# Kernel tuning notes

Measured on AMD Instinct MI355X. Metric: run time of the kernel, lower is better.

Reference implementation:

```python
import jax, jax.numpy as jnp
import numpy as np

N_CLUSTERS = 512
TEMPERATURE = 0.1


def setup_inputs() -> dict:
    key = jax.random.key(0)
    k1, k2 = jax.random.split(key)
    x = jax.random.normal(k1, (32, 1024, 256), dtype=jnp.float32)
    centroids = jax.random.normal(k2, (N_CLUSTERS, 256), dtype=jnp.float32)
    return {"x": x, "centroids": centroids}


def reference(x, centroids):
    # Flatten non-cluster axes into a sample axis: [N, D]
    B, S, D = x.shape
    xf = x.reshape(-1, D)  # [N, D]
    x_sq = jnp.sum(xf * xf, axis=-1, keepdims=True)           # [N, 1]
    c_sq = jnp.sum(centroids * centroids, axis=-1)             # [K]
    cross = jnp.einsum('nd,kd->nk', xf, centroids)             # [N, K]
    dists = x_sq - 2.0 * cross + c_sq[None, :]                 # [N, K]
    # Temperature-scaled soft assignments
    assignments = jax.nn.softmax(-dists / TEMPERATURE, axis=-1)  # [N, K]
    # Restore leading (non-feature) dims, append cluster axis
    return assignments.reshape(B, S, N_CLUSTERS)
```

## Files before the change

### kernel.cpp

```cpp
#include <hip/hip_runtime.h>

#define NROWS 32768
#define KC 512
#define DDIM 256
#define BM 64
#define BK 16
#define KCH (DDIM / BK)
#define CHUNK_USH (KC * BK)

typedef __attribute__((ext_vector_type(8)))  short bf16x8;
typedef __attribute__((ext_vector_type(16))) float f32x16;

union U8 { unsigned short u[8]; bf16x8 v; };

__device__ __forceinline__ unsigned short f2bf(float f) {
    union { float f; unsigned int u; } a; a.f = f;
    unsigned int r = a.u + 0x7fffu + ((a.u >> 16) & 1u);
    return (unsigned short)(r >> 16);
}
__device__ __forceinline__ float bf2f(unsigned short h) {
    union { unsigned int u; float f; } a; a.u = ((unsigned int)h) << 16;
    return a.f;
}

__global__ __launch_bounds__(64) void prep_c(const float* __restrict__ c,
                                             unsigned short* __restrict__ bhi,
                                             unsigned short* __restrict__ blo,
                                             float* __restrict__ csq10) {
    const int n = blockIdx.x, lane = threadIdx.x;
    const int d0 = lane * 4;
    float4 v = ((const float4*)(c + (size_t)n * DDIM))[lane];
    float vv[4] = {v.x, v.y, v.z, v.w};
    unsigned short hh[4], ll[4];
    float ssq = 0.f;
    #pragma unroll
    for (int i = 0; i < 4; ++i) {
        ssq += vv[i] * vv[i];
        hh[i] = f2bf(vv[i]);
        ll[i] = f2bf(vv[i] - bf2f(hh[i]));
    }
    #pragma unroll
    for (int off = 32; off; off >>= 1) ssq += __shfl_xor(ssq, off);
    if (lane == 0) csq10[n] = 10.f * ssq;
    const int ks = d0 >> 4;
    const int h  = (d0 >> 3) & 1;
    const int j0 = d0 & 7;
    const size_t dst = (size_t)ks * CHUNK_USH + (n >> 5) * 512 +
                       (h * 32 + (n & 31)) * 8 + j0;
    *(ushort4*)(bhi + dst) = make_ushort4(hh[0], hh[1], hh[2], hh[3]);
    *(ushort4*)(blo + dst) = make_ushort4(ll[0], ll[1], ll[2], ll[3]);
}

__global__ __launch_bounds__(256, 2) void kmeans_mfma(
    const float* __restrict__ x, const unsigned short* __restrict__ bhi,
    const unsigned short* __restrict__ blo, const float* __restrict__ csq10,
    float* __restrict__ out) {
    __shared__ float  lbuf[16 * 516];
    __shared__ float  red0[2][BM], red1[2][BM];
    __shared__ float2 MI[BM];

    const int tid  = threadIdx.x;
    const int w    = tid >> 6, lane = tid & 63;
    const int wm   = w >> 1, wn = w & 1;
    const int c5   = lane & 31, h = lane >> 5;
    const int row0 = blockIdx.x * BM;

    f32x16 acc[8];
    #pragma unroll
    for (int t = 0; t < 8; ++t)
        #pragma unroll
        for (int r = 0; r < 16; ++r) acc[t][r] = 0.f;

    const float* xrow = x + (size_t)(row0 + wm * 32 + c5) * DDIM + h * 8;
    const unsigned short* bhB = bhi + (wn * 8) * 512 + lane * 8;
    const unsigned short* blB = blo + (wn * 8) * 512 + lane * 8;

    for (int ks = 0; ks < KCH; ++ks) {
        const size_t cb = (size_t)ks * CHUNK_USH;
        bf16x8 bh[8], bl[8];
        #pragma unroll
        for (int t = 0; t < 8; ++t) bh[t] = *(const bf16x8*)(bhB + cb + t * 512);
        #pragma unroll
        for (int t = 0; t < 8; ++t) bl[t] = *(const bf16x8*)(blB + cb + t * 512);
        float4 a0 = *(const float4*)(xrow + ks * BK);
        float4 a1 = *(const float4*)(xrow + ks * BK + 4);
        __syncthreads();

        bf16x8 ah, al;
        {
            float v8[8] = {a0.x, a0.y, a0.z, a0.w, a1.x, a1.y, a1.z, a1.w};
            U8 H, L;
            #pragma unroll
            for (int i = 0; i < 8; ++i) {
                H.u[i] = f2bf(v8[i]);
                L.u[i] = f2bf(v8[i] - bf2f(H.u[i]));
            }
            ah = H.v; al = L.v;
        }
        #pragma unroll
        for (int t = 0; t < 8; ++t) {
            acc[t] = __builtin_amdgcn_mfma_f32_32x32x16_bf16(ah, bh[t], acc[t], 0, 0, 0);
            acc[t] = __builtin_amdgcn_mfma_f32_32x32x16_bf16(ah, bl[t], acc[t], 0, 0, 0);
            acc[t] = __builtin_amdgcn_mfma_f32_32x32x16_bf16(al, bh[t], acc[t], 0, 0, 0);
        }
    }

    float csqv[8];
    #pragma unroll
    for (int t = 0; t < 8; ++t) csqv[t] = csq10[wn * 256 + t * 32 + c5];

    #pragma unroll
    for (int r = 0; r < 16; ++r) {
        float pm = -1e30f;
        #pragma unroll
        for (int t = 0; t < 8; ++t) pm = fmaxf(pm, 20.f * acc[t][r] - csqv[t]);
        #pragma unroll
        for (int off = 1; off < 32; off <<= 1) pm = fmaxf(pm, __shfl_xor(pm, off));
        if (c5 == 0) red0[wn][wm * 32 + (r & 3) + 8 * (r >> 2) + 4 * h] = pm;
    }
    __syncthreads();
    #pragma unroll
    for (int r = 0; r < 16; ++r) {
        const int   row = wm * 32 + (r & 3) + 8 * (r >> 2) + 4 * h;
        const float Mf  = fmaxf(red0[0][row], red0[1][row]);
        float ps = 0.f;
        #pragma unroll
        for (int t = 0; t < 8; ++t) ps += __expf(20.f * acc[t][r] - csqv[t] - Mf);
        #pragma unroll
        for (int off = 1; off < 32; off <<= 1) ps += __shfl_xor(ps, off);
        if (c5 == 0) red1[wn][row] = ps;
    }
    __syncthreads();
    if (tid < BM) {
        const float Mf = fmaxf(red0[0][tid], red0[1][tid]);
        const float Sf = red1[0][tid] + red1[1][tid];
        MI[tid] = make_float2(Mf, 1.f / Sf);
    }
    __syncthreads();

    #pragma unroll
    for (int p = 0; p < 4; ++p) {
        if (wm == (p >> 1)) {
            #pragma unroll
            for (int i = 0; i < 8; ++i) {
                const int    rr = (p & 1) * 8 + i;
                const int    lr = (i & 3) + 8 * (i >> 2) + 4 * h;
                const float2 mi = MI[p * 16 + lr];
                #pragma unroll
                for (int t = 0; t < 8; ++t)
                    lbuf[lr * 516 + wn * 256 + t * 32 + c5] =
                        __expf(20.f * acc[t][rr] - csqv[t] - mi.x) * mi.y;
            }
        }
        __syncthreads();
        #pragma unroll
        for (int j = 0; j < 8; ++j) {
            const int f    = j * 256 + tid;
            const int lrow = f >> 7;
            const int c4   = f & 127;
            float4    v    = *(const float4*)&lbuf[lrow * 516 + c4 * 4];
            *(float4*)(out + (size_t)(row0 + p * 16 + lrow) * KC + c4 * 4) = v;
        }
        __syncthreads();
    }
}

extern "C" void kernel_launch(void* const* d_in, const int* in_sizes, int n_in,
                              void* d_out, int out_size, void* d_ws, size_t ws_size,
                              hipStream_t stream) {
    const float* x   = (const float*)d_in[0];
    const float* c   = (const float*)d_in[1];
    float*       out = (float*)d_out;

    unsigned short* bhi   = (unsigned short*)d_ws;
    unsigned short* blo   = bhi + (size_t)KCH * CHUNK_USH;
    float*          csq10 = (float*)(blo + (size_t)KCH * CHUNK_USH);

    prep_c<<<KC, 64, 0, stream>>>(c, bhi, blo, csq10);
    kmeans_mfma<<<NROWS / BM, 256, 0, stream>>>(x, bhi, blo, csq10, out);
}
```

Before: 124.8 us.

## Shrink row tile, widen block to 8 waves, stage split-bf16 x in LDS

Row tile drops from 64 to 32 and the block grows to 512 threads, so each of 8 waves covers 64 centroids of a single 32-row strip. The whole x tile is loaded once, split into hi/lo bf16 and stored in swizzled LDS, removing the per-iteration global x loads and conversions. The LDS staging buffer is unioned with the output transpose buffer, and the softmax reductions now combine across 8 waves. Each wave holds fewer accumulators, which should allow more resident waves, but every centroid fragment is now reloaded from global/L2 by twice as many blocks.

```diff
diff --git a/kernel.cpp b/kernel.cpp
--- a/kernel.cpp
+++ b/kernel.cpp
@@ -3,7 +3,7 @@
 #define NROWS 32768
 #define KC 512
 #define DDIM 256
-#define BM 64
+#define BM 32
 #define BK 16
 #define KCH (DDIM / BK)
 #define CHUNK_USH (KC * BK)
@@ -51,114 +51,136 @@
     *(ushort4*)(blo + dst) = make_ushort4(ll[0], ll[1], ll[2], ll[3]);
 }
 
-__global__ __launch_bounds__(256, 2) void kmeans_mfma(
+union SmemU {
+    unsigned short A[2][BM * 256];
+    float lbuf[16 * 516];
+};
+
+__global__ __launch_bounds__(512, 4) void kmeans_mfma(
     const float* __restrict__ x, const unsigned short* __restrict__ bhi,
     const unsigned short* __restrict__ blo, const float* __restrict__ csq10,
     float* __restrict__ out) {
-    __shared__ float  lbuf[16 * 516];
-    __shared__ float  red0[2][BM], red1[2][BM];
+    __shared__ __align__(16) SmemU sm;
+    __shared__ float  red0[8][BM], red1[8][BM];
+    __shared__ float  Mrow[BM];
     __shared__ float2 MI[BM];
 
     const int tid  = threadIdx.x;
     const int w    = tid >> 6, lane = tid & 63;
-    const int wm   = w >> 1, wn = w & 1;
     const int c5   = lane & 31, h = lane >> 5;
     const int row0 = blockIdx.x * BM;
 
-    f32x16 acc[8];
-    #pragma unroll
-    for (int t = 0; t < 8; ++t)
+    f32x16 acc[2];
+    #pragma unroll
+    for (int t = 0; t < 2; ++t)
         #pragma unroll
         for (int r = 0; r < 16; ++r) acc[t][r] = 0.f;
 
-    const float* xrow = x + (size_t)(row0 + wm * 32 + c5) * DDIM + h * 8;
-    const unsigned short* bhB = bhi + (wn * 8) * 512 + lane * 8;
-    const unsigned short* blB = blo + (wn * 8) * 512 + lane * 8;
+    {
+        const float4* x4 = (const float4*)(x + (size_t)row0 * DDIM);
+        #pragma unroll
+        for (int j = 0; j < 4; ++j) {
+            const int fidx = j * 512 + tid;
+            const int r    = fidx >> 6;
+            const int col4 = fidx & 63;
+            float4 v = x4[fidx];
+            const int o    = col4 >> 1, half = col4 & 1;
+            const int p    = o ^ r;
+            const int dst  = r * 256 + p * 8 + half * 4;
+            float vv[4] = {v.x, v.y, v.z, v.w};
+            unsigned short hh[4], ll[4];
+            #pragma unroll
+            for (int i = 0; i < 4; ++i) {
+                hh[i] = f2bf(vv[i]);
+                ll[i] = f2bf(vv[i] - bf2f(hh[i]));
+            }
+            *(ushort4*)&sm.A[0][dst] = make_ushort4(hh[0], hh[1], hh[2], hh[3]);
+            *(ushort4*)&sm.A[1][dst] = make_ushort4(ll[0], ll[1], ll[2], ll[3]);
+        }
+    }
+    __syncthreads();
+
+    const unsigned short* bhB = bhi + (size_t)(w * 2) * 512 + lane * 8;
+    const unsigned short* blB = blo + (size_t)(w * 2) * 512 + lane * 8;
 
     for (int ks = 0; ks < KCH; ++ks) {
         const size_t cb = (size_t)ks * CHUNK_USH;
-        bf16x8 bh[8], bl[8];
-        #pragma unroll
-        for (int t = 0; t < 8; ++t) bh[t] = *(const bf16x8*)(bhB + cb + t * 512);
-        #pragma unroll
-        for (int t = 0; t < 8; ++t) bl[t] = *(const bf16x8*)(blB + cb + t * 512);
-        float4 a0 = *(const float4*)(xrow + ks * BK);
-        float4 a1 = *(const float4*)(xrow + ks * BK + 4);
+        bf16x8 bh[2], bl[2];
+        #pragma unroll
+        for (int t = 0; t < 2; ++t) {
+            bh[t] = *(const bf16x8*)(bhB + cb + t * 512);
+            bl[t] = *(const bf16x8*)(blB + cb + t * 512);
+        }
+        const int po = (2 * ks + h) ^ c5;
+        bf16x8 ah = *(const bf16x8*)&sm.A[0][c5 * 256 + po * 8];
+        bf16x8 al = *(const bf16x8*)&sm.A[1][c5 * 256 + po * 8];
         __syncthreads();
 
-        bf16x8 ah, al;
-        {
-            float v8[8] = {a0.x, a0.y, a0.z, a0.w, a1.x, a1.y, a1.z, a1.w};
-            U8 H, L;
-            #pragma unroll
-            for (int i = 0; i < 8; ++i) {
-                H.u[i] = f2bf(v8[i]);
-                L.u[i] = f2bf(v8[i] - bf2f(H.u[i]));
-            }
-            ah = H.v; al = L.v;
-        }
-        #pragma unroll
-        for (int t = 0; t < 8; ++t) {
+        #pragma unroll
+        for (int t = 0; t < 2; ++t) {
             acc[t] = __builtin_amdgcn_mfma_f32_32x32x16_bf16(ah, bh[t], acc[t], 0, 0, 0);
             acc[t] = __builtin_amdgcn_mfma_f32_32x32x16_bf16(ah, bl[t], acc[t], 0, 0, 0);
             acc[t] = __builtin_amdgcn_mfma_f32_32x32x16_bf16(al, bh[t], acc[t], 0, 0, 0);
         }
     }
 
-    float csqv[8];
-    #pragma unroll
-    for (int t = 0; t < 8; ++t) csqv[t] = csq10[wn * 256 + t * 32 + c5];
+    float csqv[2];
+    #pragma unroll
+    for (int t = 0; t < 2; ++t) csqv[t] = csq10[w * 64 + t * 32 + c5];
 
     #pragma unroll
     for (int r = 0; r < 16; ++r) {
-        float pm = -1e30f;
-        #pragma unroll
-        for (int t = 0; t < 8; ++t) pm = fmaxf(pm, 20.f * acc[t][r] - csqv[t]);
+        float pm = fmaxf(20.f * acc[0][r] - csqv[0], 20.f * acc[1][r] - csqv[1]);
         #pragma unroll
         for (int off = 1; off < 32; off <<= 1) pm = fmaxf(pm, __shfl_xor(pm, off));
-        if (c5 == 0) red0[wn][wm * 32 + (r & 3) + 8 * (r >> 2) + 4 * h] = pm;
+        if (c5 == 0) red0[w][(r & 3) + 8 * (r >> 2) + 4 * h] = pm;
+    }
+    __syncthreads();
+    if (tid < BM) {
+        float m = -1e30f;
+        #pragma unroll
+        for (int ww = 0; ww < 8; ++ww) m = fmaxf(m, red0[ww][tid]);
+        Mrow[tid] = m;
     }
     __syncthreads();
     #pragma unroll
     for (int r = 0; r < 16; ++r) {
-        const int   row = wm * 32 + (r & 3) + 8 * (r >> 2) + 4 * h;
-        const float Mf  = fmaxf(red0[0][row], red0[1][row]);
-        float ps = 0.f;
-        #pragma unroll
-        for (int t = 0; t < 8; ++t) ps += __expf(20.f * acc[t][r] - csqv[t] - Mf);
+        const int   row = (r & 3) + 8 * (r >> 2) + 4 * h;
+        const float Mf  = Mrow[row];
+        float ps = __expf(20.f * acc[0][r] - csqv[0] - Mf) +
+                   __expf(20.f * acc[1][r] - csqv[1] - Mf);
         #pragma unroll
         for (int off = 1; off < 32; off <<= 1) ps += __shfl_xor(ps, off);
-        if (c5 == 0) red1[wn][row] = ps;
+        if (c5 == 0) red1[w][row] = ps;
     }
     __syncthreads();
     if (tid < BM) {
-        const float Mf = fmaxf(red0[0][tid], red0[1][tid]);
-        const float Sf = red1[0][tid] + red1[1][tid];
-        MI[tid] = make_float2(Mf, 1.f / Sf);
-    }
-    __syncthreads();
-
-    #pragma unroll
-    for (int p = 0; p < 4; ++p) {
-        if (wm == (p >> 1)) {
+        float s = 0.f;
+        #pragma unroll
+        for (int ww = 0; ww < 8; ++ww) s += red1[ww][tid];
+        MI[tid] = make_float2(Mrow[tid], 1.f / s);
+    }
+    __syncthreads();
+
+    #pragma unroll
+    for (int p = 0; p < 2; ++p) {
+        #pragma unroll
+        for (int i = 0; i < 8; ++i) {
+            const int    r  = p * 8 + i;
+            const int    lr = (r & 3) + 8 * ((r >> 2) & 1) + 4 * h;
+            const float2 mi = MI[p * 16 + lr];
             #pragma unroll
-            for (int i = 0; i < 8; ++i) {
-                const int    rr = (p & 1) * 8 + i;
-                const int    lr = (i & 3) + 8 * (i >> 2) + 4 * h;
-                const float2 mi = MI[p * 16 + lr];
-                #pragma unroll
-                for (int t = 0; t < 8; ++t)
-                    lbuf[lr * 516 + wn * 256 + t * 32 + c5] =
-                        __expf(20.f * acc[t][rr] - csqv[t] - mi.x) * mi.y;
-            }
+            for (int t = 0; t < 2; ++t)
+                sm.lbuf[lr * 516 + w * 64 + t * 32 + c5] =
+                    __expf(20.f * acc[t][r] - csqv[t] - mi.x) * mi.y;
         }
         __syncthreads();
         #pragma unroll
-        for (int j = 0; j < 8; ++j) {
-            const int f    = j * 256 + tid;
+        for (int j = 0; j < 4; ++j) {
+            const int f    = j * 512 + tid;
             const int lrow = f >> 7;
             const int c4   = f & 127;
-            float4    v    = *(const float4*)&lbuf[lrow * 516 + c4 * 4];
+            float4    v    = *(const float4*)&sm.lbuf[lrow * 516 + c4 * 4];
             *(float4*)(out + (size_t)(row0 + p * 16 + lrow) * KC + c4 * 4) = v;
         }
         __syncthreads();
@@ -177,5 +199,5 @@
     float*          csq10 = (float*)(blo + (size_t)KCH * CHUNK_USH);
 
     prep_c<<<KC, 64, 0, stream>>>(c, bhi, blo, csq10);
-    kmeans_mfma<<<NROWS / BM, 256, 0, stream>>>(x, bhi, blo, csq10, out);
-}
+    kmeans_mfma<<<NROWS / BM, 512, 0, stream>>>(x, bhi, blo, csq10, out);
+}
```

After: 126.2 us. No clear change (+1.1%).
